# Performance work log

Measured on AMD Instinct MI355X. Metric: run time of the kernel, lower is better.

The kernel has to match this reference:

```python
import jax, jax.numpy as jnp
import numpy as np

B, D, L = 16384, 1024, 4


def setup_inputs() -> dict:
    key = jax.random.key(0)
    ks = jax.random.split(key, 5)
    scale = 1.0 / np.sqrt(D)
    x = jax.random.normal(ks[0], (B, D), dtype=jnp.float32)
    # torch nn.Linear default init: U(-1/sqrt(fan_in), 1/sqrt(fan_in))
    Ws = jax.random.uniform(ks[1], (L, D, D), jnp.float32, -scale, scale)
    bs = jax.random.uniform(ks[2], (L, D), jnp.float32, -scale, scale)
    Wo = jax.random.uniform(ks[3], (D, D), jnp.float32, -scale, scale)
    bo = jax.random.uniform(ks[4], (D,), jnp.float32, -scale, scale)
    return {"x": x, "Ws": Ws, "bs": bs, "Wo": Wo, "bo": bo}


def reference(x, Ws, bs, Wo, bo):
    # torch: matmul(x[:, :, None], x[:, None, :]).sum(2) == x * x.sum(-1, keepdims=True)
    interactions = jax.nn.relu(x * jnp.sum(x, axis=-1, keepdims=True))  # (B, D)
    h = x
    for i in range(L):  # fixed small layer count
        h = jax.nn.relu(h @ Ws[i].T + bs[i])  # torch Linear: y = x W^T + b
    out = ((h + interactions) * 0.5) @ Wo.T + bo
    return out
```

## Files before the change

kernel.cpp:

```cpp
#include <hip/hip_runtime.h>


#define DDIM 1024
#define BROWS 16384
#define NLAYERS 4

typedef __attribute__((ext_vector_type(8))) short s8v;
typedef __attribute__((ext_vector_type(4))) float f4v;

__device__ __forceinline__ unsigned short f2bf(float f) {
    unsigned int u = __float_as_uint(f);
    u += 0x7fffu + ((u >> 16) & 1u);
    return (unsigned short)(u >> 16);
}

__device__ __forceinline__ void gld16(const void* g, void* l) {
    __builtin_amdgcn_global_load_lds(
        (const __attribute__((address_space(1))) unsigned int*)g,
        (__attribute__((address_space(3))) unsigned int*)l, 16, 0, 0);
}

__global__ __launch_bounds__(256) void prep_kernel(
    const float* __restrict__ x, unsigned short* __restrict__ xb,
    float* __restrict__ rowsum)
{
    const int row = blockIdx.x;
    const int t = threadIdx.x;
    const float4 v = *(const float4*)(x + (size_t)row * DDIM + t * 4);
    ushort4 o;
    o.x = f2bf(v.x); o.y = f2bf(v.y); o.z = f2bf(v.z); o.w = f2bf(v.w);
    *(ushort4*)(xb + (size_t)row * DDIM + t * 4) = o;
    float s = v.x + v.y + v.z + v.w;
    #pragma unroll
    for (int off = 32; off > 0; off >>= 1) s += __shfl_down(s, off, 64);
    __shared__ float red[4];
    const int wave = t >> 6, lane = t & 63;
    if (lane == 0) red[wave] = s;
    __syncthreads();
    if (t == 0) rowsum[row] = red[0] + red[1] + red[2] + red[3];
}

__global__ __launch_bounds__(256) void cvt_kernel(
    const float* __restrict__ in, unsigned short* __restrict__ out, int n)
{
    const int i = (blockIdx.x * 256 + threadIdx.x) * 4;
    if (i < n) {
        const float4 v = *(const float4*)(in + i);
        ushort4 o;
        o.x = f2bf(v.x); o.y = f2bf(v.y); o.z = f2bf(v.z); o.w = f2bf(v.w);
        *(ushort4*)(out + i) = o;
    }
}

template <int MODE>
__global__ __launch_bounds__(256, 2) void gemm_bt(
    const unsigned short* __restrict__ A,
    const unsigned short* __restrict__ Bw,
    const float* __restrict__ bias,
    void* __restrict__ out,
    const float* __restrict__ xf,
    const float* __restrict__ rowsum,
    int M, int N, int K)
{
    constexpr int BM = 128, BN = 128, BK = 32;
    __shared__ unsigned short sA[BM * BK];
    __shared__ unsigned short sB[BN * BK];

    const int t = threadIdx.x;
    const int wave = t >> 6, lane = t & 63;
    const int wm = wave & 1, wn = wave >> 1;
    const int rowBase = blockIdx.x * BM;
    const int colBase = blockIdx.y * BN;

    f4v acc[4][4] = {};

    const int c0r = t >> 2,         c0k = (t & 3) * 8;
    const int c1r = (t + 256) >> 2, c1k = ((t + 256) & 3) * 8;

    for (int kt = 0; kt < K; kt += BK) {
        if (kt) __syncthreads();
        gld16(A  + (size_t)(rowBase + c0r) * K + kt + c0k, (char*)sA + t * 16);
        gld16(Bw + (size_t)(colBase + c0r) * K + kt + c0k, (char*)sB + t * 16);
        gld16(A  + (size_t)(rowBase + c1r) * K + kt + c1k, (char*)sA + (t + 256) * 16);
        gld16(Bw + (size_t)(colBase + c1r) * K + kt + c1k, (char*)sB + (t + 256) * 16);
        __syncthreads();

        const int mrow = lane & 15;
        const int koff = (lane >> 4) * 8;
        s8v af[4], bfr[4];
        #pragma unroll
        for (int mi = 0; mi < 4; ++mi)
            af[mi] = *(const s8v*)&sA[(wm * 64 + mi * 16 + mrow) * BK + koff];
        #pragma unroll
        for (int ni = 0; ni < 4; ++ni)
            bfr[ni] = *(const s8v*)&sB[(wn * 64 + ni * 16 + mrow) * BK + koff];
        #pragma unroll
        for (int mi = 0; mi < 4; ++mi)
            #pragma unroll
            for (int ni = 0; ni < 4; ++ni)
                acc[mi][ni] = __builtin_amdgcn_mfma_f32_16x16x32_bf16(
                    af[mi], bfr[ni], acc[mi][ni], 0, 0, 0);
    }

    const int nlane = lane & 15;
    const int rbase = (lane >> 4) * 4;
    #pragma unroll
    for (int ni = 0; ni < 4; ++ni) {
        const int n = colBase + wn * 64 + ni * 16 + nlane;
        const float bv = bias[n];
        #pragma unroll
        for (int mi = 0; mi < 4; ++mi) {
            const int mbase = rowBase + wm * 64 + mi * 16 + rbase;
            #pragma unroll
            for (int r = 0; r < 4; ++r) {
                const int row = mbase + r;
                float v = acc[mi][ni][r] + bv;
                if (MODE == 0) {
                    v = v > 0.f ? v : 0.f;
                    ((unsigned short*)out)[(size_t)row * N + n] = f2bf(v);
                } else if (MODE == 1) {
                    v = v > 0.f ? v : 0.f;
                    float it = xf[(size_t)row * N + n] * rowsum[row];
                    it = it > 0.f ? it : 0.f;
                    ((unsigned short*)out)[(size_t)row * N + n] = f2bf(0.5f * (v + it));
                } else {
                    ((float*)out)[(size_t)row * N + n] = v;
                }
            }
        }
    }
}

extern "C" void kernel_launch(void* const* d_in, const int* in_sizes, int n_in,
                              void* d_out, int out_size, void* d_ws, size_t ws_size,
                              hipStream_t stream) {
    const float* x  = (const float*)d_in[0];
    const float* Ws = (const float*)d_in[1];
    const float* bs = (const float*)d_in[2];
    const float* Wo = (const float*)d_in[3];
    const float* bo = (const float*)d_in[4];
    float* out = (float*)d_out;

    char* ws = (char*)d_ws;
    unsigned short* xb  = (unsigned short*)(ws);
    unsigned short* h0  = (unsigned short*)(ws + 33554432);
    unsigned short* h1  = (unsigned short*)(ws + 67108864);
    unsigned short* wb  = (unsigned short*)(ws + 100663296);
    unsigned short* wob = (unsigned short*)(ws + 109051904);
    float*          rsm = (float*)(ws + 111149056);

    prep_kernel<<<BROWS, 256, 0, stream>>>(x, xb, rsm);
    cvt_kernel<<<(NLAYERS * DDIM * DDIM) / 1024, 256, 0, stream>>>(
        Ws, wb, NLAYERS * DDIM * DDIM);
    cvt_kernel<<<(DDIM * DDIM) / 1024, 256, 0, stream>>>(Wo, wob, DDIM * DDIM);

    dim3 g(BROWS / 128, DDIM / 128);
    gemm_bt<0><<<g, 256, 0, stream>>>(xb, wb,                 bs,            h0, nullptr, nullptr, BROWS, DDIM, DDIM);
    gemm_bt<0><<<g, 256, 0, stream>>>(h0, wb + 1 * DDIM * DDIM, bs + 1 * DDIM, h1, nullptr, nullptr, BROWS, DDIM, DDIM);
    gemm_bt<0><<<g, 256, 0, stream>>>(h1, wb + 2 * DDIM * DDIM, bs + 2 * DDIM, h0, nullptr, nullptr, BROWS, DDIM, DDIM);
    gemm_bt<1><<<g, 256, 0, stream>>>(h0, wb + 3 * DDIM * DDIM, bs + 3 * DDIM, h1, x, rsm, BROWS, DDIM, DDIM);
    gemm_bt<2><<<g, 256, 0, stream>>>(h1, wob,                bo,            out, nullptr, nullptr, BROWS, DDIM, DDIM);
}
```

Baseline: 371.7 us.

## Fuse all five MLP layers into one kernel keeping activations in LDS

Replaces the prep kernel and five separate GEMM launches with a single persistent-per-row-block kernel. Each block holds a 64-row activation tile (padded stride) in shared memory across all layers and reads bf16 weights directly from global/L2 into registers. This removes the round trips of intermediate activations through HBM and the extra launches. The cost is that every block streams the full weight matrices with no LDS staging, only 256 blocks exist, and the 132KB LDS tile limits occupancy, so weight-load latency may dominate.

```diff
diff --git a/kernel.cpp b/kernel.cpp
--- a/kernel.cpp
+++ b/kernel.cpp
@@ -3,7 +3,7 @@
 
 #define DDIM 1024
 #define BROWS 16384
-#define NLAYERS 4
+#define HSTR 1032
 
 typedef __attribute__((ext_vector_type(8))) short s8v;
 typedef __attribute__((ext_vector_type(4))) float f4v;
@@ -12,32 +12,6 @@
     unsigned int u = __float_as_uint(f);
     u += 0x7fffu + ((u >> 16) & 1u);
     return (unsigned short)(u >> 16);
-}
-
-__device__ __forceinline__ void gld16(const void* g, void* l) {
-    __builtin_amdgcn_global_load_lds(
-        (const __attribute__((address_space(1))) unsigned int*)g,
-        (__attribute__((address_space(3))) unsigned int*)l, 16, 0, 0);
-}
-
-__global__ __launch_bounds__(256) void prep_kernel(
-    const float* __restrict__ x, unsigned short* __restrict__ xb,
-    float* __restrict__ rowsum)
-{
-    const int row = blockIdx.x;
-    const int t = threadIdx.x;
-    const float4 v = *(const float4*)(x + (size_t)row * DDIM + t * 4);
-    ushort4 o;
-    o.x = f2bf(v.x); o.y = f2bf(v.y); o.z = f2bf(v.z); o.w = f2bf(v.w);
-    *(ushort4*)(xb + (size_t)row * DDIM + t * 4) = o;
-    float s = v.x + v.y + v.z + v.w;
-    #pragma unroll
-    for (int off = 32; off > 0; off >>= 1) s += __shfl_down(s, off, 64);
-    __shared__ float red[4];
-    const int wave = t >> 6, lane = t & 63;
-    if (lane == 0) red[wave] = s;
-    __syncthreads();
-    if (t == 0) rowsum[row] = red[0] + red[1] + red[2] + red[3];
 }
 
 __global__ __launch_bounds__(256) void cvt_kernel(
@@ -52,79 +26,108 @@
     }
 }
 
-template <int MODE>
-__global__ __launch_bounds__(256, 2) void gemm_bt(
-    const unsigned short* __restrict__ A,
-    const unsigned short* __restrict__ Bw,
-    const float* __restrict__ bias,
-    void* __restrict__ out,
-    const float* __restrict__ xf,
-    const float* __restrict__ rowsum,
-    int M, int N, int K)
+__global__ __launch_bounds__(512, 2) void fused_kernel(
+    const float* __restrict__ x,
+    const unsigned short* __restrict__ Wb,
+    const float* __restrict__ bs,
+    const unsigned short* __restrict__ Wob,
+    const float* __restrict__ bo,
+    float* __restrict__ out)
 {
-    constexpr int BM = 128, BN = 128, BK = 32;
-    __shared__ unsigned short sA[BM * BK];
-    __shared__ unsigned short sB[BN * BK];
+    __shared__ unsigned short h[64 * HSTR];
+    __shared__ float rs[64];
 
     const int t = threadIdx.x;
-    const int wave = t >> 6, lane = t & 63;
-    const int wm = wave & 1, wn = wave >> 1;
-    const int rowBase = blockIdx.x * BM;
-    const int colBase = blockIdx.y * BN;
+    const int lane = t & 63;
+    const int wave = t >> 6;
+    const int rowBase = blockIdx.x * 64;
 
-    f4v acc[4][4] = {};
+    {
+        const int r = t >> 3;
+        const int cseg = (t & 7) * 128;
+        const float* xr = x + (size_t)(rowBase + r) * DDIM + cseg;
+        float s = 0.f;
+        for (int c = 0; c < 128; c += 4) {
+            const float4 v = *(const float4*)(xr + c);
+            s += v.x + v.y + v.z + v.w;
+            ushort4 o;
+            o.x = f2bf(v.x); o.y = f2bf(v.y); o.z = f2bf(v.z); o.w = f2bf(v.w);
+            *(ushort4*)&h[r * HSTR + cseg + c] = o;
+        }
+        s += __shfl_down(s, 4);
+        s += __shfl_down(s, 2);
+        s += __shfl_down(s, 1);
+        if ((t & 7) == 0) rs[r] = s;
+    }
+    __syncthreads();
 
-    const int c0r = t >> 2,         c0k = (t & 3) * 8;
-    const int c1r = (t + 256) >> 2, c1k = ((t + 256) & 3) * 8;
+    const int colW = wave * 128;
+    const int mrow = lane & 15;
+    const int kq   = lane >> 4;
+    const int quad = lane >> 4;
 
-    for (int kt = 0; kt < K; kt += BK) {
-        if (kt) __syncthreads();
-        gld16(A  + (size_t)(rowBase + c0r) * K + kt + c0k, (char*)sA + t * 16);
-        gld16(Bw + (size_t)(colBase + c0r) * K + kt + c0k, (char*)sB + t * 16);
-        gld16(A  + (size_t)(rowBase + c1r) * K + kt + c1k, (char*)sA + (t + 256) * 16);
-        gld16(Bw + (size_t)(colBase + c1r) * K + kt + c1k, (char*)sB + (t + 256) * 16);
+    #pragma unroll 1
+    for (int layer = 0; layer < 5; ++layer) {
+        const unsigned short* W = (layer == 4) ? Wob : Wb + (size_t)layer * DDIM * DDIM;
+        const float* bias = (layer == 4) ? bo : bs + (size_t)layer * DDIM;
+
+        f4v acc[4][8] = {};
+
+        const unsigned short* wbase = W + (size_t)(colW + mrow) * DDIM + kq * 8;
+
+        for (int k0 = 0; k0 < DDIM; k0 += 32) {
+            s8v bfr[8];
+            #pragma unroll
+            for (int ni = 0; ni < 8; ++ni)
+                bfr[ni] = *(const s8v*)(wbase + (size_t)ni * 16 * DDIM + k0);
+            s8v af[4];
+            #pragma unroll
+            for (int mi = 0; mi < 4; ++mi)
+                af[mi] = *(const s8v*)&h[(mi * 16 + mrow) * HSTR + k0 + kq * 8];
+            #pragma unroll
+            for (int mi = 0; mi < 4; ++mi)
+                #pragma unroll
+                for (int ni = 0; ni < 8; ++ni)
+                    acc[mi][ni] = __builtin_amdgcn_mfma_f32_16x16x32_bf16(
+                        af[mi], bfr[ni], acc[mi][ni], 0, 0, 0);
+        }
+
         __syncthreads();
 
-        const int mrow = lane & 15;
-        const int koff = (lane >> 4) * 8;
-        s8v af[4], bfr[4];
-        #pragma unroll
-        for (int mi = 0; mi < 4; ++mi)
-            af[mi] = *(const s8v*)&sA[(wm * 64 + mi * 16 + mrow) * BK + koff];
-        #pragma unroll
-        for (int ni = 0; ni < 4; ++ni)
-            bfr[ni] = *(const s8v*)&sB[(wn * 64 + ni * 16 + mrow) * BK + koff];
-        #pragma unroll
-        for (int mi = 0; mi < 4; ++mi)
+        if (layer < 4) {
             #pragma unroll
-            for (int ni = 0; ni < 4; ++ni)
-                acc[mi][ni] = __builtin_amdgcn_mfma_f32_16x16x32_bf16(
-                    af[mi], bfr[ni], acc[mi][ni], 0, 0, 0);
-    }
-
-    const int nlane = lane & 15;
-    const int rbase = (lane >> 4) * 4;
-    #pragma unroll
-    for (int ni = 0; ni < 4; ++ni) {
-        const int n = colBase + wn * 64 + ni * 16 + nlane;
-        const float bv = bias[n];
-        #pragma unroll
-        for (int mi = 0; mi < 4; ++mi) {
-            const int mbase = rowBase + wm * 64 + mi * 16 + rbase;
+            for (int ni = 0; ni < 8; ++ni) {
+                const int n = colW + ni * 16 + mrow;
+                const float bv = bias[n];
+                #pragma unroll
+                for (int mi = 0; mi < 4; ++mi) {
+                    #pragma unroll
+                    for (int r = 0; r < 4; ++r) {
+                        const int row = mi * 16 + quad * 4 + r;
+                        float v = acc[mi][ni][r] + bv;
+                        v = v > 0.f ? v : 0.f;
+                        if (layer == 3) {
+                            float it = x[(size_t)(rowBase + row) * DDIM + n] * rs[row];
+                            it = it > 0.f ? it : 0.f;
+                            v = 0.5f * (v + it);
+                        }
+                        h[row * HSTR + n] = f2bf(v);
+                    }
+                }
+            }
+            __syncthreads();
+        } else {
             #pragma unroll
-            for (int r = 0; r < 4; ++r) {
-                const int row = mbase + r;
-                float v = acc[mi][ni][r] + bv;
-                if (MODE == 0) {
-                    v = v > 0.f ? v : 0.f;
-                    ((unsigned short*)out)[(size_t)row * N + n] = f2bf(v);
-                } else if (MODE == 1) {
-                    v = v > 0.f ? v : 0.f;
-                    float it = xf[(size_t)row * N + n] * rowsum[row];
-                    it = it > 0.f ? it : 0.f;
-                    ((unsigned short*)out)[(size_t)row * N + n] = f2bf(0.5f * (v + it));
-                } else {
-                    ((float*)out)[(size_t)row * N + n] = v;
+            for (int ni = 0; ni < 8; ++ni) {
+                const int n = colW + ni * 16 + mrow;
+                const float bv = bias[n];
+                #pragma unroll
+                for (int mi = 0; mi < 4; ++mi) {
+                    #pragma unroll
+                    for (int r = 0; r < 4; ++r) {
+                        const int row = mi * 16 + quad * 4 + r;
+                        out[(size_t)(rowBase + row) * DDIM + n] = acc[mi][ni][r] + bv;
+                    }
                 }
             }
         }
@@ -142,22 +145,11 @@
     float* out = (float*)d_out;
 
     char* ws = (char*)d_ws;
-    unsigned short* xb  = (unsigned short*)(ws);
-    unsigned short* h0  = (unsigned short*)(ws + 33554432);
-    unsigned short* h1  = (unsigned short*)(ws + 67108864);
-    unsigned short* wb  = (unsigned short*)(ws + 100663296);
-    unsigned short* wob = (unsigned short*)(ws + 109051904);
-    float*          rsm = (float*)(ws + 111149056);
+    unsigned short* wb  = (unsigned short*)(ws);
+    unsigned short* wob = (unsigned short*)(ws + 8388608);
 
-    prep_kernel<<<BROWS, 256, 0, stream>>>(x, xb, rsm);
-    cvt_kernel<<<(NLAYERS * DDIM * DDIM) / 1024, 256, 0, stream>>>(
-        Ws, wb, NLAYERS * DDIM * DDIM);
+    cvt_kernel<<<(4 * DDIM * DDIM) / 1024, 256, 0, stream>>>(Ws, wb, 4 * DDIM * DDIM);
     cvt_kernel<<<(DDIM * DDIM) / 1024, 256, 0, stream>>>(Wo, wob, DDIM * DDIM);
 
-    dim3 g(BROWS / 128, DDIM / 128);
-    gemm_bt<0><<<g, 256, 0, stream>>>(xb, wb,                 bs,            h0, nullptr, nullptr, BROWS, DDIM, DDIM);
-    gemm_bt<0><<<g, 256, 0, stream>>>(h0, wb + 1 * DDIM * DDIM, bs + 1 * DDIM, h1, nullptr, nullptr, BROWS, DDIM, DDIM);
-    gemm_bt<0><<<g, 256, 0, stream>>>(h1, wb + 2 * DDIM * DDIM, bs + 2 * DDIM, h0, nullptr, nullptr, BROWS, DDIM, DDIM);
-    gemm_bt<1><<<g, 256, 0, stream>>>(h0, wb + 3 * DDIM * DDIM, bs + 3 * DDIM, h1, x, rsm, BROWS, DDIM, DDIM);
-    gemm_bt<2><<<g, 256, 0, stream>>>(h1, wob,                bo,            out, nullptr, nullptr, BROWS, DDIM, DDIM);
+    fused_kernel<<<BROWS / 64, 512, 0, stream>>>(x, wb, bs, wob, bo, out);
 }
```

Result: slower. 470.9 us (+26.7%).

## Double K-step per barrier, stage bf16 epilogue through LDS, merge weight conversions

Applied to the files above, without the earlier changes.

The GEMM main loop now loads a 64-wide K slab (two 32-wide sub-tiles) per barrier pair, which halves the number of synchronisations. The bf16 epilogues write the tile to shared memory and then emit coalesced 16-byte row stores. The interaction term now reads the bf16 copy of x instead of fp32 x, which cuts epilogue traffic but lowers precision of that term. The two weight-conversion launches are merged into one, and M/N/K are made compile-time constants.

```diff
diff --git a/kernel.cpp b/kernel.cpp
--- a/kernel.cpp
+++ b/kernel.cpp
@@ -3,7 +3,6 @@
 
 #define DDIM 1024
 #define BROWS 16384
-#define NLAYERS 4
 
 typedef __attribute__((ext_vector_type(8))) short s8v;
 typedef __attribute__((ext_vector_type(4))) float f4v;
@@ -13,7 +12,9 @@
     u += 0x7fffu + ((u >> 16) & 1u);
     return (unsigned short)(u >> 16);
 }
-
+__device__ __forceinline__ float bf2f(unsigned short u) {
+    return __uint_as_float(((unsigned int)u) << 16);
+}
 __device__ __forceinline__ void gld16(const void* g, void* l) {
     __builtin_amdgcn_global_load_lds(
         (const __attribute__((address_space(1))) unsigned int*)g,
@@ -41,15 +42,15 @@
 }
 
 __global__ __launch_bounds__(256) void cvt_kernel(
-    const float* __restrict__ in, unsigned short* __restrict__ out, int n)
+    const float* __restrict__ Ws, const float* __restrict__ Wo,
+    unsigned short* __restrict__ out)
 {
     const int i = (blockIdx.x * 256 + threadIdx.x) * 4;
-    if (i < n) {
-        const float4 v = *(const float4*)(in + i);
-        ushort4 o;
-        o.x = f2bf(v.x); o.y = f2bf(v.y); o.z = f2bf(v.z); o.w = f2bf(v.w);
-        *(ushort4*)(out + i) = o;
-    }
+    const float* src = (i < 4 * DDIM * DDIM) ? (Ws + i) : (Wo + (i - 4 * DDIM * DDIM));
+    const float4 v = *(const float4*)src;
+    ushort4 o;
+    o.x = f2bf(v.x); o.y = f2bf(v.y); o.z = f2bf(v.z); o.w = f2bf(v.w);
+    *(ushort4*)(out + i) = o;
 }
 
 template <int MODE>
@@ -58,75 +59,107 @@
     const unsigned short* __restrict__ Bw,
     const float* __restrict__ bias,
     void* __restrict__ out,
-    const float* __restrict__ xf,
-    const float* __restrict__ rowsum,
-    int M, int N, int K)
+    const unsigned short* __restrict__ xb,
+    const float* __restrict__ rowsum)
 {
-    constexpr int BM = 128, BN = 128, BK = 32;
-    __shared__ unsigned short sA[BM * BK];
-    __shared__ unsigned short sB[BN * BK];
+    constexpr int K = DDIM, N = DDIM;
+    __shared__ unsigned short smem[4][128 * 32];
 
     const int t = threadIdx.x;
     const int wave = t >> 6, lane = t & 63;
     const int wm = wave & 1, wn = wave >> 1;
-    const int rowBase = blockIdx.x * BM;
-    const int colBase = blockIdx.y * BN;
+    const int rowBase = blockIdx.x * 128;
+    const int colBase = blockIdx.y * 128;
 
     f4v acc[4][4] = {};
 
-    const int c0r = t >> 2,         c0k = (t & 3) * 8;
-    const int c1r = (t + 256) >> 2, c1k = ((t + 256) & 3) * 8;
+    const int c0r = t >> 2, c0k = (t & 3) * 8;
+    const int mrow = lane & 15;
+    const int koff = (lane >> 4) * 8;
 
-    for (int kt = 0; kt < K; kt += BK) {
+    for (int kt = 0; kt < K; kt += 64) {
         if (kt) __syncthreads();
-        gld16(A  + (size_t)(rowBase + c0r) * K + kt + c0k, (char*)sA + t * 16);
-        gld16(Bw + (size_t)(colBase + c0r) * K + kt + c0k, (char*)sB + t * 16);
-        gld16(A  + (size_t)(rowBase + c1r) * K + kt + c1k, (char*)sA + (t + 256) * 16);
-        gld16(Bw + (size_t)(colBase + c1r) * K + kt + c1k, (char*)sB + (t + 256) * 16);
+        const unsigned short* a0 = A  + (size_t)(rowBase + c0r) * K + kt + c0k;
+        const unsigned short* b0 = Bw + (size_t)(colBase + c0r) * K + kt + c0k;
+        gld16(a0,               (char*)smem[0] + t * 16);
+        gld16(a0 + 64 * K,      (char*)smem[0] + (t + 256) * 16);
+        gld16(b0,               (char*)smem[2] + t * 16);
+        gld16(b0 + 64 * K,      (char*)smem[2] + (t + 256) * 16);
+        gld16(a0 + 32,          (char*)smem[1] + t * 16);
+        gld16(a0 + 64 * K + 32, (char*)smem[1] + (t + 256) * 16);
+        gld16(b0 + 32,          (char*)smem[3] + t * 16);
+        gld16(b0 + 64 * K + 32, (char*)smem[3] + (t + 256) * 16);
         __syncthreads();
 
-        const int mrow = lane & 15;
-        const int koff = (lane >> 4) * 8;
-        s8v af[4], bfr[4];
         #pragma unroll
-        for (int mi = 0; mi < 4; ++mi)
-            af[mi] = *(const s8v*)&sA[(wm * 64 + mi * 16 + mrow) * BK + koff];
-        #pragma unroll
-        for (int ni = 0; ni < 4; ++ni)
-            bfr[ni] = *(const s8v*)&sB[(wn * 64 + ni * 16 + mrow) * BK + koff];
-        #pragma unroll
-        for (int mi = 0; mi < 4; ++mi)
+        for (int s = 0; s < 2; ++s) {
+            s8v af[4], bfr[4];
+            #pragma unroll
+            for (int mi = 0; mi < 4; ++mi)
+                af[mi] = *(const s8v*)&smem[s][(wm * 64 + mi * 16 + mrow) * 32 + koff];
             #pragma unroll
             for (int ni = 0; ni < 4; ++ni)
-                acc[mi][ni] = __builtin_amdgcn_mfma_f32_16x16x32_bf16(
-                    af[mi], bfr[ni], acc[mi][ni], 0, 0, 0);
+                bfr[ni] = *(const s8v*)&smem[2 + s][(wn * 64 + ni * 16 + mrow) * 32 + koff];
+            #pragma unroll
+            for (int mi = 0; mi < 4; ++mi)
+                #pragma unroll
+                for (int ni = 0; ni < 4; ++ni)
+                    acc[mi][ni] = __builtin_amdgcn_mfma_f32_16x16x32_bf16(
+                        af[mi], bfr[ni], acc[mi][ni], 0, 0, 0);
+        }
     }
 
-    const int nlane = lane & 15;
-    const int rbase = (lane >> 4) * 4;
-    #pragma unroll
-    for (int ni = 0; ni < 4; ++ni) {
-        const int n = colBase + wn * 64 + ni * 16 + nlane;
-        const float bv = bias[n];
+    const int quad = lane >> 4;
+    if (MODE == 2) {
+        float* o = (float*)out;
         #pragma unroll
-        for (int mi = 0; mi < 4; ++mi) {
-            const int mbase = rowBase + wm * 64 + mi * 16 + rbase;
+        for (int ni = 0; ni < 4; ++ni) {
+            const int n = colBase + wn * 64 + ni * 16 + mrow;
+            const float bv = bias[n];
             #pragma unroll
-            for (int r = 0; r < 4; ++r) {
-                const int row = mbase + r;
-                float v = acc[mi][ni][r] + bv;
-                if (MODE == 0) {
+            for (int mi = 0; mi < 4; ++mi)
+                #pragma unroll
+                for (int r = 0; r < 4; ++r) {
+                    const int row = rowBase + wm * 64 + mi * 16 + quad * 4 + r;
+                    o[(size_t)row * N + n] = acc[mi][ni][r] + bv;
+                }
+        }
+    } else {
+        __syncthreads();
+        unsigned short* sC = (unsigned short*)smem;
+        #pragma unroll
+        for (int ni = 0; ni < 4; ++ni) {
+            const int n = wn * 64 + ni * 16 + mrow;
+            const float bv = bias[colBase + n];
+            #pragma unroll
+            for (int mi = 0; mi < 4; ++mi)
+                #pragma unroll
+                for (int r = 0; r < 4; ++r) {
+                    const int row = wm * 64 + mi * 16 + quad * 4 + r;
+                    float v = acc[mi][ni][r] + bv;
                     v = v > 0.f ? v : 0.f;
-                    ((unsigned short*)out)[(size_t)row * N + n] = f2bf(v);
-                } else if (MODE == 1) {
-                    v = v > 0.f ? v : 0.f;
-                    float it = xf[(size_t)row * N + n] * rowsum[row];
+                    sC[row * 128 + n] = f2bf(v);
+                }
+        }
+        __syncthreads();
+        unsigned short* o16 = (unsigned short*)out;
+        #pragma unroll
+        for (int i = 0; i < 8; ++i) {
+            const int idx = t + i * 256;
+            const int row = idx >> 4, ch = idx & 15;
+            s8v c = *(const s8v*)&sC[row * 128 + ch * 8];
+            if (MODE == 1) {
+                const float rsv = rowsum[rowBase + row];
+                const s8v xv = *(const s8v*)&xb[(size_t)(rowBase + row) * DDIM + colBase + ch * 8];
+                #pragma unroll
+                for (int j = 0; j < 8; ++j) {
+                    float it = bf2f((unsigned short)xv[j]) * rsv;
                     it = it > 0.f ? it : 0.f;
-                    ((unsigned short*)out)[(size_t)row * N + n] = f2bf(0.5f * (v + it));
-                } else {
-                    ((float*)out)[(size_t)row * N + n] = v;
+                    const float v = 0.5f * (bf2f((unsigned short)c[j]) + it);
+                    c[j] = (short)f2bf(v);
                 }
             }
+            *(s8v*)&o16[(size_t)(rowBase + row) * DDIM + colBase + ch * 8] = c;
         }
     }
 }
@@ -146,18 +179,16 @@
     unsigned short* h0  = (unsigned short*)(ws + 33554432);
     unsigned short* h1  = (unsigned short*)(ws + 67108864);
     unsigned short* wb  = (unsigned short*)(ws + 100663296);
-    unsigned short* wob = (unsigned short*)(ws + 109051904);
     float*          rsm = (float*)(ws + 111149056);
 
     prep_kernel<<<BROWS, 256, 0, stream>>>(x, xb, rsm);
-    cvt_kernel<<<(NLAYERS * DDIM * DDIM) / 1024, 256, 0, stream>>>(
-        Ws, wb, NLAYERS * DDIM * DDIM);
-    cvt_kernel<<<(DDIM * DDIM) / 1024, 256, 0, stream>>>(Wo, wob, DDIM * DDIM);
+    cvt_kernel<<<(5 * DDIM * DDIM) / 1024, 256, 0, stream>>>(Ws, Wo, wb);
 
+    const size_t WSZ = (size_t)DDIM * DDIM;
     dim3 g(BROWS / 128, DDIM / 128);
-    gemm_bt<0><<<g, 256, 0, stream>>>(xb, wb,                 bs,            h0, nullptr, nullptr, BROWS, DDIM, DDIM);
-    gemm_bt<0><<<g, 256, 0, stream>>>(h0, wb + 1 * DDIM * DDIM, bs + 1 * DDIM, h1, nullptr, nullptr, BROWS, DDIM, DDIM);
-    gemm_bt<0><<<g, 256, 0, stream>>>(h1, wb + 2 * DDIM * DDIM, bs + 2 * DDIM, h0, nullptr, nullptr, BROWS, DDIM, DDIM);
-    gemm_bt<1><<<g, 256, 0, stream>>>(h0, wb + 3 * DDIM * DDIM, bs + 3 * DDIM, h1, x, rsm, BROWS, DDIM, DDIM);
-    gemm_bt<2><<<g, 256, 0, stream>>>(h1, wob,                bo,            out, nullptr, nullptr, BROWS, DDIM, DDIM);
+    gemm_bt<0><<<g, 256, 0, stream>>>(xb, wb,           bs,            h0, nullptr, nullptr);
+    gemm_bt<0><<<g, 256, 0, stream>>>(h0, wb + 1 * WSZ, bs + 1 * DDIM, h1, nullptr, nullptr);
+    gemm_bt<0><<<g, 256, 0, stream>>>(h1, wb + 2 * WSZ, bs + 2 * DDIM, h0, nullptr, nullptr);
+    gemm_bt<1><<<g, 256, 0, stream>>>(h0, wb + 3 * WSZ, bs + 3 * DDIM, h1, xb, rsm);
+    gemm_bt<2><<<g, 256, 0, stream>>>(h1, wb + 4 * WSZ, bo,            out, nullptr, nullptr);
 }
```

After: 373.4 us. Within noise of the previous version (+0.4%).
